# Kernel optimization log

Measured on AMD Instinct MI355X. Metric: run time of the kernel, lower is better.

Reference implementation:

```python
import jax, jax.numpy as jnp
import numpy as np

B, L, HID, NH, HD = 2, 2048, 1024, 16, 64


def _positions_and_segs(lengths):
    # lengths: (L,) int64, sub-sequence lengths packed at front, zeros pad.
    cs = jnp.cumsum(lengths)                       # (L,) segment end offsets
    t = jnp.arange(lengths.shape[0])
    seg = jnp.searchsorted(cs, t, side='right')    # segment id per token
    seg = jnp.minimum(seg, lengths.shape[0] - 1)
    starts = cs - lengths                          # segment start offsets
    pos = t - starts[seg]                          # position reset per segment
    valid = t < cs[-1]
    return jnp.where(valid, pos, 0), seg, valid


def _rope(x, positions):
    # x: (B, L, H, D); positions: (B, L)
    d = x.shape[-1]
    inv_freq = 1.0 / (10000.0 ** (jnp.arange(0, d, 2, dtype=jnp.float32) / d))
    freqs = positions[..., None].astype(jnp.float32) * inv_freq   # (B, L, d/2)
    emb = jnp.concatenate([freqs, freqs], axis=-1)                # (B, L, d)
    cos = jnp.cos(emb)[:, :, None, :]
    sin = jnp.sin(emb)[:, :, None, :]
    x1, x2 = jnp.split(x, 2, axis=-1)
    rot = jnp.concatenate([-x2, x1], axis=-1)
    return x * cos + rot * sin


def setup_inputs() -> dict:
    key = jax.random.key(0)
    ks = jax.random.split(key, 5)
    hidden_states = jax.random.normal(ks[0], (B, L, HID), dtype=jnp.float32)
    aml = np.zeros((B, L), dtype=np.int64)
    aml[0, :3] = [512, 768, 520]    # sums to 1800 (248 padding tokens)
    aml[1, :3] = [1024, 512, 512]   # sums to 2048 (no padding)
    attention_mask_in_length = jnp.asarray(aml)
    Wqkv = jax.random.normal(ks[1], (HID, 3 * HID), dtype=jnp.float32) * 0.02
    bqkv = jax.random.normal(ks[2], (3 * HID,), dtype=jnp.float32) * 0.02
    Wout = jax.random.normal(ks[3], (HID, HID), dtype=jnp.float32) * 0.02
    bout = jax.random.normal(ks[4], (HID,), dtype=jnp.float32) * 0.02
    return {"hidden_states": hidden_states,
            "attention_mask_in_length": attention_mask_in_length,
            "Wqkv": Wqkv, "bqkv": bqkv, "Wout": Wout, "bout": bout}


def reference(hidden_states, attention_mask_in_length, Wqkv, bqkv, Wout, bout):
    Bb, Ll, _ = hidden_states.shape
    qkv = hidden_states @ Wqkv + bqkv                 # (B, L, 3*HID)
    qkv = qkv.reshape(Bb, Ll, 3, NH, HD)
    q, k, v = qkv[:, :, 0], qkv[:, :, 1], qkv[:, :, 2]
    scale = HD ** -0.5
    q = q * scale  # module pre-scales q before RoPE
    positions, seg, valid = jax.vmap(_positions_and_segs)(attention_mask_in_length)
    q = _rope(q, positions)
    k = _rope(k, positions)
    # block-diagonal attention: only within same sub-sequence, valid tokens
    mask = (seg[:, :, None] == seg[:, None, :]) & valid[:, :, None] & valid[:, None, :]
    # flash_attn with softmax_scale=None applies head_dim**-0.5 again (faithful)
    scores = jnp.einsum('bihd,bjhd->bhij', q, k) * scale
    scores = jnp.where(mask[:, None, :, :], scores, -1e9)
    probs = jax.nn.softmax(scores, axis=-1)
    out = jnp.einsum('bhij,bjhd->bihd', probs, v)     # (B, L, H, D)
    out = jnp.where(valid[:, :, None, None], out, 0.0)  # pad_input zeros padding rows
    out = out.reshape(Bb, Ll, NH * HD)
    return out @ Wout + bout
```

## Files before the change

kernel.cpp:

```cpp
#include <hip/hip_runtime.h>
#include <math.h>

#define B_ 2
#define L_ 2048
#define HID_ 1024
#define NH_ 16
#define HD_ 64
#define QBLK 128

typedef unsigned short u16;
typedef __attribute__((ext_vector_type(8))) _Float16 half8;
typedef __attribute__((ext_vector_type(4))) float f32x4;

__device__ __forceinline__ u16 f2h(float x) {
    _Float16 h = (_Float16)x; u16 r; __builtin_memcpy(&r, &h, 2); return r;
}
__device__ __forceinline__ float fexp2(float x) {
    float r;
    asm("v_exp_f32 %0, %1" : "=v"(r) : "v"(x));
    return r;
}
__device__ __forceinline__ unsigned pkrtz(float a, float b) {
    auto v = __builtin_amdgcn_cvt_pkrtz(a, b);
    unsigned r; __builtin_memcpy(&r, &v, 4); return r;
}
__device__ __forceinline__ void gload16(const void* g, void* l) {
    __builtin_amdgcn_global_load_lds(
        (const __attribute__((address_space(1))) void*)g,
        (__attribute__((address_space(3))) void*)l, 16, 0, 0);
}

__global__ void setup_kernel(const int* __restrict__ aml,
                             int* __restrict__ sstart, int* __restrict__ send,
                             int* __restrict__ poss_out)
{
    const int b = blockIdx.x;
    const int tid = threadIdx.x;
    __shared__ int cs[L_];
    __shared__ int partial[256];

    int vals[8];
    const int t0 = tid * 8;
    int s = 0;
#pragma unroll
    for (int e = 0; e < 8; ++e) { vals[e] = aml[b * L_ + t0 + e]; s += vals[e]; }
    partial[tid] = s;
    __syncthreads();
    if (tid == 0) {
        int acc = 0;
        for (int i = 0; i < 256; ++i) { int tmp = partial[i]; partial[i] = acc; acc += tmp; }
    }
    __syncthreads();
    int off = partial[tid];
#pragma unroll
    for (int e = 0; e < 8; ++e) { off += vals[e]; cs[t0 + e] = off; }
    __syncthreads();

    const int total = cs[L_ - 1];
    for (int t = tid; t < L_; t += 256) {
        int lo = 0, hi = L_;
        while (lo < hi) { int mid = (lo + hi) >> 1; if (cs[mid] <= t) lo = mid + 1; else hi = mid; }
        int seg = lo < (L_ - 1) ? lo : (L_ - 1);
        int end = cs[seg];
        int len = aml[b * L_ + seg];
        int start = end - len;
        bool valid = t < total;
        poss_out[b * L_ + t] = valid ? (t - start) : 0;
        sstart[b * L_ + t] = valid ? start : 0x7fffffff;
        send[b * L_ + t]   = valid ? end : 0;
    }
}

__global__ void conv_all(const float* __restrict__ hidden, u16* __restrict__ hidh,
                         const float* __restrict__ Wqkv, u16* __restrict__ wqh,
                         const float* __restrict__ Wout, u16* __restrict__ woh,
                         const int* __restrict__ poss,
                         float* __restrict__ ctab, float* __restrict__ stab)
{
    __shared__ float t[32][33];
    const int bid = blockIdx.x;
    const int tid = threadIdx.x;
    if (bid < 4096) {
        int i = (bid * 256 + tid) * 4;
        float4 v = *(const float4*)&hidden[i];
        *(ushort4*)&hidh[i] = make_ushort4(f2h(v.x), f2h(v.y), f2h(v.z), f2h(v.w));
        return;
    }
    if (bid >= 8192) {
        const double kexp = 13.287712379549449 / 32.0;
        int idx = (bid - 8192) * 256 + tid;
        int d = idx & 31;
        int bt = idx >> 5;
        double f = (double)poss[bt] * exp2(-(double)d * kexp);
        ctab[idx] = (float)cos(f);
        stab[idx] = (float)sin(f);
        return;
    }
    const float* W; u16* o; int Kd = 1024, Nd, n0, k0;
    if (bid < 7168) {
        int idx = bid - 4096; W = Wqkv; o = wqh; Nd = 3072;
        n0 = (idx % 96) * 32; k0 = (idx / 96) * 32;
    } else {
        int idx = bid - 7168; W = Wout; o = woh; Nd = 1024;
        n0 = (idx & 31) * 32; k0 = (idx >> 5) * 32;
    }
    const int r = tid >> 5, c = tid & 31;
#pragma unroll
    for (int i = 0; i < 4; ++i)
        t[r + 8 * i][c] = W[(size_t)(k0 + r + 8 * i) * Nd + n0 + c];
    __syncthreads();
#pragma unroll
    for (int i = 0; i < 4; ++i)
        o[(size_t)(n0 + r + 8 * i) * Kd + k0 + c] = f2h(t[c][r + 8 * i]);
}

template <int MODE>
__global__ __launch_bounds__(256, 3)
void gemm_mfma(const u16* __restrict__ Ap, const u16* __restrict__ Bp,
               const float* __restrict__ bias, float* __restrict__ C,
               u16* __restrict__ qb, u16* __restrict__ kb, u16* __restrict__ vtb,
               const float* __restrict__ ctab, const float* __restrict__ stab,
               int M, int N, int K)
{
    __shared__ u16 Asl[128 * 64];
    __shared__ u16 Bsl[128 * 64];

    const int tid = threadIdx.x;
    const int wave = tid >> 6, lane = tid & 63;

    const int nwg = gridDim.x * gridDim.y;
    const int bid = blockIdx.y * gridDim.x + blockIdx.x;
    const int cpx = nwg >> 3;
    const int swz = (bid & 7) * cpx + (bid >> 3);
    const int brow = (swz / gridDim.x) * 128;
    const int bcol = (swz % gridDim.x) * 128;

    const int wr = (wave >> 1) * 64, wc = (wave & 1) * 64;
    const int grow = tid >> 3, gslot = tid & 7;
    const int fr = lane & 15, kg = lane >> 4;

    f32x4 acc[4][4];
#pragma unroll
    for (int m = 0; m < 4; ++m)
#pragma unroll
        for (int n = 0; n < 4; ++n) acc[m][n] = (f32x4){0.f, 0.f, 0.f, 0.f};

    for (int ka = 0; ka < K; ka += 64) {
#pragma unroll
        for (int c = 0; c < 4; ++c) {
            int row = c * 32 + grow;
            int sg = gslot ^ (row & 7);
            gload16(&Ap[(size_t)(brow + row) * K + ka + sg * 8],
                    (char*)Asl + c * 4096 + wave * 1024);
            gload16(&Bp[(size_t)(bcol + row) * K + ka + sg * 8],
                    (char*)Bsl + c * 4096 + wave * 1024);
        }
        __syncthreads();

#pragma unroll
        for (int kk = 0; kk < 2; ++kk) {
            half8 af[4], bfv[4];
            const int cbase = kk * 4 + kg;
#pragma unroll
            for (int n = 0; n < 4; ++n) {
                int r = wc + n * 16 + fr;
                bfv[n] = *(const half8*)&Bsl[r * 64 + ((cbase ^ (r & 7)) << 3)];
            }
#pragma unroll
            for (int m = 0; m < 4; ++m) {
                int r = wr + m * 16 + fr;
                af[m] = *(const half8*)&Asl[r * 64 + ((cbase ^ (r & 7)) << 3)];
            }
#pragma unroll
            for (int m = 0; m < 4; ++m)
#pragma unroll
                for (int n = 0; n < 4; ++n)
                    acc[m][n] = __builtin_amdgcn_mfma_f32_16x16x32_f16(
                        af[m], bfv[n], acc[m][n], 0, 0, 0);
        }
        __syncthreads();
    }

    const int cr = (lane >> 4) * 4;
    const int cc = lane & 15;
    if (MODE == 0) {
#pragma unroll
        for (int m = 0; m < 4; ++m) {
#pragma unroll
            for (int n = 0; n < 4; ++n) {
                const int col = bcol + wc + n * 16 + cc;
                const float bv = bias[col];
                const int row0 = brow + wr + m * 16 + cr;
#pragma unroll
                for (int rg = 0; rg < 4; ++rg)
                    C[(size_t)(row0 + rg) * N + col] = acc[m][n][rg] + bv;
            }
        }
    } else {
        const int colbase = bcol + wc;
        const int sel = colbase >> 10;
        const int hh = (colbase & 1023) >> 6;
#pragma unroll
        for (int m = 0; m < 4; ++m) {
            const int row0 = brow + wr + m * 16 + cr;
            const int bidx = row0 >> 11, t0 = row0 & (L_ - 1);
            if (sel == 2) {
#pragma unroll
                for (int n = 0; n < 4; ++n) {
                    int col = colbase + n * 16 + cc;
                    float bv = bias[col];
                    int d = col & 63;
                    ushort4 pk = make_ushort4(
                        f2h(acc[m][n][0] + bv), f2h(acc[m][n][1] + bv),
                        f2h(acc[m][n][2] + bv), f2h(acc[m][n][3] + bv));
                    *(ushort4*)&vtb[((((size_t)bidx * NH_ + hh) * HD_) + d) * L_ + t0] = pk;
                }
            } else {
                u16* dst = (sel == 0) ? qb : kb;
#pragma unroll
                for (int np = 0; np < 2; ++np) {
                    int col1 = colbase + np * 16 + cc;
                    int d1 = np * 16 + cc;
                    float bv1 = bias[col1], bv2 = bias[col1 + 32];
#pragma unroll
                    for (int rg = 0; rg < 4; ++rg) {
                        int t = t0 + rg;
                        float c = ctab[((size_t)bidx * L_ + t) * 32 + d1];
                        float s = stab[((size_t)bidx * L_ + t) * 32 + d1];
                        float x1 = acc[m][np][rg] + bv1;
                        float x2 = acc[m][np + 2][rg] + bv2;
                        size_t base = ((((size_t)bidx * NH_ + hh) * L_) + t) * (size_t)HD_;
                        dst[base + d1]      = f2h(x1 * c - x2 * s);
                        dst[base + d1 + 32] = f2h(x2 * c + x1 * s);
                    }
                }
            }
        }
    }
}

__global__ __launch_bounds__(512)
void attn_mfma(const u16* __restrict__ qb, const u16* __restrict__ kbuf,
               const u16* __restrict__ vt, const int* __restrict__ sstart,
               const int* __restrict__ send, u16* __restrict__ ohi)
{
    __shared__ u16 Ksb[2][64 * 64];
    __shared__ u16 Vsb[3][64 * 64];
    __shared__ u16 Pw[8 * 2 * 16 * 64];
    __shared__ int ss[QBLK], se[QBLK];

    const int b = blockIdx.z, h = blockIdx.y, q0 = blockIdx.x * QBLK;
    const int tid = threadIdx.x, wave = tid >> 6, lane = tid & 63;
    const int fr = lane & 15, kg = lane >> 4;
    const size_t hb = (((size_t)b * NH_) + h) * (size_t)(L_ * HD_);
    const size_t hv = (((size_t)b * NH_) + h) * (size_t)(HD_ * L_);

    if (tid < QBLK) { ss[tid] = sstart[b * L_ + q0 + tid]; se[tid] = send[b * L_ + q0 + tid]; }

    const u16* qrow = &qb[hb + (size_t)(q0 + wave * 16 + fr) * HD_ + kg * 8];
    half8 qf0 = *(const half8*)(qrow);
    half8 qf1 = *(const half8*)(qrow + 32);
    __syncthreads();

    int kmin = 0x7fffffff, kmax = 0;
#pragma unroll 8
    for (int r = 0; r < QBLK; ++r) { kmin = min(kmin, ss[r]); kmax = max(kmax, se[r]); }

    const int myss_ = ss[wave * 16 + fr];
    const int myse_ = se[wave * 16 + fr];

    float l_ = 0.f;
    f32x4 oacc[4];
#pragma unroll
    for (int i = 0; i < 4; ++i) oacc[i] = (f32x4){0.f, 0.f, 0.f, 0.f};

    const int grow = tid >> 3;
    const int sg = (tid & 7) ^ (grow & 7);
    const float SCL = 0.015625f * 1.4426950408889634f;
    const int fx = fr & 7;

    const int kt_first = kmin & ~63;
    const int ntile = (kmax > kt_first) ? ((kmax - kt_first + 63) >> 6) : 0;

    if (ntile > 0) {
        gload16(&kbuf[hb + (size_t)(kt_first + grow) * HD_ + sg * 8],
                (char*)Ksb[0] + wave * 1024);
        gload16(&vt[hv + (size_t)grow * L_ + kt_first + sg * 8],
                (char*)Vsb[0] + wave * 1024);
    }
    __syncthreads();

    for (int i = 0; i < ntile; ++i) {
        const int kt0 = kt_first + i * 64;
        const u16* Ks = Ksb[i & 1];

        f32x4 sc4[4];
#pragma unroll
        for (int ct = 0; ct < 4; ++ct) sc4[ct] = (f32x4){0.f, 0.f, 0.f, 0.f};
        __builtin_amdgcn_s_setprio(1);
#pragma unroll
        for (int kk = 0; kk < 2; ++kk) {
            half8 qf = kk ? qf1 : qf0;
#pragma unroll
            for (int ct = 0; ct < 4; ++ct) {
                int r = ct * 16 + fr;
                half8 kf = *(const half8*)&Ks[r * 64 + (((kk * 4 + kg) ^ (r & 7)) << 3)];
                sc4[ct] = __builtin_amdgcn_mfma_f32_16x16x32_f16(kf, qf, sc4[ct], 0, 0, 0);
            }
        }
        __builtin_amdgcn_s_setprio(0);

        if (i + 1 < ntile) {
            const int ktn = kt0 + 64;
            gload16(&kbuf[hb + (size_t)(ktn + grow) * HD_ + sg * 8],
                    (char*)Ksb[(i + 1) & 1] + wave * 1024);
            gload16(&vt[hv + (size_t)grow * L_ + ktn + sg * 8],
                    (char*)Vsb[(i + 1) % 3] + wave * 1024);
        }

        if (i > 0) {
            const u16* Vsp = Vsb[(i - 1) % 3];
            const u16* pwr = &Pw[((wave << 1) + ((i - 1) & 1)) * 1024 + fr * 64];
            __builtin_amdgcn_s_setprio(1);
#pragma unroll
            for (int ks2 = 0; ks2 < 2; ++ks2) {
                half8 pf = *(const half8*)&pwr[((4 * ks2 + kg) ^ fx) << 3];
#pragma unroll
                for (int dt = 0; dt < 4; ++dt) {
                    int r = dt * 16 + fr;
                    half8 vf = *(const half8*)&Vsp[r * 64 + (((ks2 * 4 + kg) ^ (r & 7)) << 3)];
                    oacc[dt] = __builtin_amdgcn_mfma_f32_16x16x32_f16(vf, pf, oacc[dt], 0, 0, 0);
                }
            }
            __builtin_amdgcn_s_setprio(0);
        }

        float p[4][4];
        float psum = 0.f;
        if (__all((kt0 >= myss_) && (kt0 + 64 <= myse_))) {
#pragma unroll
            for (int ct = 0; ct < 4; ++ct)
#pragma unroll
                for (int reg = 0; reg < 4; ++reg) {
                    float e = fexp2(sc4[ct][reg] * SCL);
                    p[ct][reg] = e;
                    psum += e;
                }
        } else {
            const int ktb = kt0 + kg * 4;
#pragma unroll
            for (int ct = 0; ct < 4; ++ct)
#pragma unroll
                for (int reg = 0; reg < 4; ++reg) {
                    int kt = ktb + ct * 16 + reg;
                    bool v = (kt >= myss_) && (kt < myse_);
                    float e = fexp2(sc4[ct][reg] * SCL);
                    p[ct][reg] = v ? e : 0.f;
                    psum += p[ct][reg];
                }
        }
        psum += __shfl_xor(psum, 16);
        psum += __shfl_xor(psum, 32);
        l_ += psum;

        u16* pww = &Pw[((wave << 1) + (i & 1)) * 1024 + fr * 64];
#pragma unroll
        for (int ct = 0; ct < 4; ++ct) {
            uint2 w;
            w.x = pkrtz(p[ct][0], p[ct][1]);
            w.y = pkrtz(p[ct][2], p[ct][3]);
            *(uint2*)&pww[(((2 * ct + (kg >> 1)) ^ fx) << 3) + (kg & 1) * 4] = w;
        }

        __syncthreads();
    }

    if (ntile > 0) {
        const int i = ntile;
        const u16* Vsp = Vsb[(i - 1) % 3];
        const u16* pwr = &Pw[((wave << 1) + ((i - 1) & 1)) * 1024 + fr * 64];
#pragma unroll
        for (int ks2 = 0; ks2 < 2; ++ks2) {
            half8 pf = *(const half8*)&pwr[((4 * ks2 + kg) ^ fx) << 3];
#pragma unroll
            for (int dt = 0; dt < 4; ++dt) {
                int r = dt * 16 + fr;
                half8 vf = *(const half8*)&Vsp[r * 64 + (((ks2 * 4 + kg) ^ (r & 7)) << 3)];
                oacc[dt] = __builtin_amdgcn_mfma_f32_16x16x32_f16(vf, pf, oacc[dt], 0, 0, 0);
            }
        }
    }

    const int t = q0 + wave * 16 + fr;
    const float inv = (myss_ < myse_) ? 1.f / l_ : 0.f;
    const size_t rowbase = ((size_t)b * L_ + t) * (size_t)HID_ + h * HD_ + kg * 4;
#pragma unroll
    for (int dt = 0; dt < 4; ++dt) {
        *(ushort4*)&ohi[rowbase + dt * 16] = make_ushort4(
            f2h(oacc[dt][0] * inv), f2h(oacc[dt][1] * inv),
            f2h(oacc[dt][2] * inv), f2h(oacc[dt][3] * inv));
    }
}

extern "C" void kernel_launch(void* const* d_in, const int* in_sizes, int n_in,
                              void* d_out, int out_size, void* d_ws, size_t ws_size,
                              hipStream_t stream)
{
    (void)in_sizes; (void)n_in; (void)out_size; (void)ws_size;
    const float* hidden = (const float*)d_in[0];
    const int*   aml    = (const int*)d_in[1];
    const float* Wqkv   = (const float*)d_in[2];
    const float* bqkv   = (const float*)d_in[3];
    const float* Wout   = (const float*)d_in[4];
    const float* bout   = (const float*)d_in[5];
    float* out = (float*)d_out;

    const size_t per = (size_t)B_ * NH_ * L_ * HD_;
    float* ctab = (float*)d_ws;
    float* stab = ctab + (size_t)B_ * L_ * 32;
    int* sstart = (int*)(stab + (size_t)B_ * L_ * 32);
    int* send   = sstart + B_ * L_;
    int* poss   = send + B_ * L_;
    u16* qbf  = (u16*)(poss + B_ * L_);
    u16* kbf  = qbf + per;
    u16* vtb  = kbf + per;
    u16* hidh = vtb + per;
    u16* wqh  = hidh + (size_t)4096 * 1024;
    u16* woh  = wqh + (size_t)3072 * 1024;

    setup_kernel<<<dim3(B_), dim3(256), 0, stream>>>(aml, sstart, send, poss);

    conv_all<<<dim3(8704), dim3(256), 0, stream>>>(hidden, hidh, Wqkv, wqh,
                                                   Wout, woh, poss, ctab, stab);

    gemm_mfma<1><<<dim3(24, 32), dim3(256), 0, stream>>>(
        hidh, wqh, bqkv, nullptr, qbf, kbf, vtb, ctab, stab,
        B_ * L_, 3 * HID_, HID_);

    attn_mfma<<<dim3(L_ / QBLK, NH_, B_), dim3(512), 0, stream>>>(
        qbf, kbf, vtb, sstart, send, hidh);

    gemm_mfma<0><<<dim3(8, 32), dim3(256), 0, stream>>>(
        hidh, woh, bout, out, nullptr, nullptr, nullptr, nullptr, nullptr,
        B_ * L_, HID_, HID_);
}
```

Measured before the change: 108.7 us.

## Triple-buffer K/V loads and compute PV in the same iteration

Deepens the K/V prefetch from one tile ahead to two by adding a third K buffer and issuing loads for tile i+2. Each iteration waits on the vmcnt counter before a raw s_barrier, in place of a __syncthreads at the end of the loop. The deferred PV MFMA of the previous tile is replaced by an immediate PV on the current tile, using a single per-wave P buffer, and the post-loop tail is removed. The aim is more latency hiding for global loads and simpler synchronization. In exchange it gives up the overlap of softmax with the previous tile's PV, and it relies on manual waitcnt accounting being correct for the gload16 LDS-direct loads.

```diff
diff --git a/kernel.cpp b/kernel.cpp
--- a/kernel.cpp
+++ b/kernel.cpp
@@ -244,9 +244,9 @@
                const u16* __restrict__ vt, const int* __restrict__ sstart,
                const int* __restrict__ send, u16* __restrict__ ohi)
 {
-    __shared__ u16 Ksb[2][64 * 64];
+    __shared__ u16 Ksb[3][64 * 64];
     __shared__ u16 Vsb[3][64 * 64];
-    __shared__ u16 Pw[8 * 2 * 16 * 64];
+    __shared__ u16 Pw[8 * 16 * 64];
     __shared__ int ss[QBLK], se[QBLK];
 
     const int b = blockIdx.z, h = blockIdx.y, q0 = blockIdx.x * QBLK;
@@ -278,6 +278,7 @@
     const int sg = (tid & 7) ^ (grow & 7);
     const float SCL = 0.015625f * 1.4426950408889634f;
     const int fx = fr & 7;
+    u16* pwl = &Pw[wave * 1024 + fr * 64];
 
     const int kt_first = kmin & ~63;
     const int ntile = (kmax > kt_first) ? ((kmax - kt_first + 63) >> 6) : 0;
@@ -288,11 +289,35 @@
         gload16(&vt[hv + (size_t)grow * L_ + kt_first + sg * 8],
                 (char*)Vsb[0] + wave * 1024);
     }
+    if (ntile > 1) {
+        gload16(&kbuf[hb + (size_t)(kt_first + 64 + grow) * HD_ + sg * 8],
+                (char*)Ksb[1] + wave * 1024);
+        gload16(&vt[hv + (size_t)grow * L_ + kt_first + 64 + sg * 8],
+                (char*)Vsb[1] + wave * 1024);
+    }
     __syncthreads();
 
     for (int i = 0; i < ntile; ++i) {
         const int kt0 = kt_first + i * 64;
-        const u16* Ks = Ksb[i & 1];
+
+        if (i + 1 < ntile) {
+            asm volatile("s_waitcnt vmcnt(2)" ::: "memory");
+        } else {
+            asm volatile("s_waitcnt vmcnt(0)" ::: "memory");
+        }
+        __builtin_amdgcn_sched_barrier(0);
+        __builtin_amdgcn_s_barrier();
+
+        if (i + 2 < ntile) {
+            const int ktn = kt0 + 128;
+            gload16(&kbuf[hb + (size_t)(ktn + grow) * HD_ + sg * 8],
+                    (char*)Ksb[(i + 2) % 3] + wave * 1024);
+            gload16(&vt[hv + (size_t)grow * L_ + ktn + sg * 8],
+                    (char*)Vsb[(i + 2) % 3] + wave * 1024);
+        }
+
+        const u16* Ks = Ksb[i % 3];
+        const u16* Vs = Vsb[i % 3];
 
         f32x4 sc4[4];
 #pragma unroll
@@ -309,31 +334,6 @@
             }
         }
         __builtin_amdgcn_s_setprio(0);
-
-        if (i + 1 < ntile) {
-            const int ktn = kt0 + 64;
-            gload16(&kbuf[hb + (size_t)(ktn + grow) * HD_ + sg * 8],
-                    (char*)Ksb[(i + 1) & 1] + wave * 1024);
-            gload16(&vt[hv + (size_t)grow * L_ + ktn + sg * 8],
-                    (char*)Vsb[(i + 1) % 3] + wave * 1024);
-        }
-
-        if (i > 0) {
-            const u16* Vsp = Vsb[(i - 1) % 3];
-            const u16* pwr = &Pw[((wave << 1) + ((i - 1) & 1)) * 1024 + fr * 64];
-            __builtin_amdgcn_s_setprio(1);
-#pragma unroll
-            for (int ks2 = 0; ks2 < 2; ++ks2) {
-                half8 pf = *(const half8*)&pwr[((4 * ks2 + kg) ^ fx) << 3];
-#pragma unroll
-                for (int dt = 0; dt < 4; ++dt) {
-                    int r = dt * 16 + fr;
-                    half8 vf = *(const half8*)&Vsp[r * 64 + (((ks2 * 4 + kg) ^ (r & 7)) << 3)];
-                    oacc[dt] = __builtin_amdgcn_mfma_f32_16x16x32_f16(vf, pf, oacc[dt], 0, 0, 0);
-                }
-            }
-            __builtin_amdgcn_s_setprio(0);
-        }
 
         float p[4][4];
         float psum = 0.f;
@@ -363,32 +363,26 @@
         psum += __shfl_xor(psum, 32);
         l_ += psum;
 
-        u16* pww = &Pw[((wave << 1) + (i & 1)) * 1024 + fr * 64];
 #pragma unroll
         for (int ct = 0; ct < 4; ++ct) {
             uint2 w;
             w.x = pkrtz(p[ct][0], p[ct][1]);
             w.y = pkrtz(p[ct][2], p[ct][3]);
-            *(uint2*)&pww[(((2 * ct + (kg >> 1)) ^ fx) << 3) + (kg & 1) * 4] = w;
-        }
-
-        __syncthreads();
-    }
-
-    if (ntile > 0) {
-        const int i = ntile;
-        const u16* Vsp = Vsb[(i - 1) % 3];
-        const u16* pwr = &Pw[((wave << 1) + ((i - 1) & 1)) * 1024 + fr * 64];
+            *(uint2*)&pwl[(((2 * ct + (kg >> 1)) ^ fx) << 3) + (kg & 1) * 4] = w;
+        }
+
+        __builtin_amdgcn_s_setprio(1);
 #pragma unroll
         for (int ks2 = 0; ks2 < 2; ++ks2) {
-            half8 pf = *(const half8*)&pwr[((4 * ks2 + kg) ^ fx) << 3];
+            half8 pf = *(const half8*)&pwl[((4 * ks2 + kg) ^ fx) << 3];
 #pragma unroll
             for (int dt = 0; dt < 4; ++dt) {
                 int r = dt * 16 + fr;
-                half8 vf = *(const half8*)&Vsp[r * 64 + (((ks2 * 4 + kg) ^ (r & 7)) << 3)];
+                half8 vf = *(const half8*)&Vs[r * 64 + (((ks2 * 4 + kg) ^ (r & 7)) << 3)];
                 oacc[dt] = __builtin_amdgcn_mfma_f32_16x16x32_f16(vf, pf, oacc[dt], 0, 0, 0);
             }
         }
+        __builtin_amdgcn_s_setprio(0);
     }
 
     const int t = q0 + wave * 16 + fr;
```

After: 108.0 us. About the same (-0.7%).
